# Kernel tuning notes

Measured on AMD Instinct MI355X. Metric: run time of the kernel, lower is better.

## Reference

```python
import jax, jax.numpy as jnp
import numpy as np

ANGLE_BITS = 3          # TurboQuantConfig.angle_bits default
LEVELS = 2 ** ANGLE_BITS
PI = np.pi


def _angle_ranges(d_minus_1, dtype):
    # hyperspherical coords: first d-2 angles in [0, pi], last angle in [0, 2*pi)
    return jnp.concatenate([
        jnp.full((d_minus_1 - 1,), PI, dtype),
        jnp.full((1,), 2.0 * PI, dtype),
    ])


def polar_compress(x):
    """x: [..., d] -> (r [...,1], theta_indices int32 [..., d-1])."""
    # suffix norms s_i = ||x[i:]|| via reversed cumsum of squares
    suffix = jnp.sqrt(jnp.cumsum((x * x)[..., ::-1], axis=-1)[..., ::-1])
    r = suffix[..., :1]
    cos_t = jnp.clip(x[..., :-1] / jnp.maximum(suffix[..., :-1], 1e-12), -1.0, 1.0)
    theta = jnp.arccos(cos_t)                      # [..., d-1], in [0, pi]
    # last angle carries the sign of x[..., -1]: map to [0, 2*pi)
    last = jnp.where(x[..., -1:] < 0, 2.0 * PI - theta[..., -1:], theta[..., -1:])
    theta = jnp.concatenate([theta[..., :-1], last], axis=-1)
    ranges = _angle_ranges(theta.shape[-1], theta.dtype)
    idx = jnp.round(theta / ranges * (LEVELS - 1)).astype(jnp.int32)
    return r, idx


def polar_decompress(r, idx):
    """(r [...,1], idx [..., d-1]) -> x_hat [..., d] via trig products."""
    d1 = idx.shape[-1]
    ranges = _angle_ranges(d1, r.dtype)
    theta = idx.astype(r.dtype) / (LEVELS - 1) * ranges
    sinp = jnp.cumprod(jnp.sin(theta), axis=-1)                 # [..., d-1]
    prods = jnp.concatenate([jnp.ones_like(r), sinp], axis=-1)  # [..., d]
    coss = jnp.concatenate([jnp.cos(theta), jnp.ones_like(r)], axis=-1)
    return r * prods * coss


def setup_inputs() -> dict:
    key = jax.random.key(0)
    kq, kk, kv, kn = jax.random.split(key, 4)
    B, H, T, k, d = 1, 32, 8192, 16, 128
    return {
        "queries": jax.random.normal(kq, (B, H, k, d), jnp.float32),
        "keys": jax.random.normal(kk, (B, H, T, d), jnp.float32),
        "values": jax.random.normal(kv, (B, H, T, d), jnp.float32),
        # faithful stand-in for `torch.randn_like(scores) * 0.01` QJL correction,
        # materialized deterministically as an input
        "qjl_noise": jax.random.normal(kn, (B, H, k, T), jnp.float32) * 0.01,
    }


def reference(queries, keys, values, qjl_noise):
    d = queries.shape[-1]
    # compress_kv_cache: polar angle quantization of keys and values
    r_k, idx_k = polar_compress(keys)
    r_v, idx_v = polar_compress(values)
    # compute_attention_with_compressed_kv: decompress-then-attend
    keys_polar = polar_decompress(r_k, idx_k)      # [B,H,T,d]
    values_polar = polar_decompress(r_v, idx_v)    # [B,H,T,d]
    scores = jnp.einsum('bhkd,bhtd->bhkt', queries, keys_polar) / jnp.sqrt(
        jnp.asarray(d, queries.dtype))
    scores = scores + qjl_noise
    attn = jax.nn.softmax(scores, axis=-1)
    return jnp.einsum('bhkt,bhtd->bhkd', attn, values_polar)
```

## Files before the change

kernel.cpp:

```cpp
#include <hip/hip_runtime.h>
#include <math.h>

typedef __attribute__((ext_vector_type(8))) short bf16x8;
typedef __attribute__((ext_vector_type(4))) float f32x4;
typedef __attribute__((ext_vector_type(2))) float f32x2;

#define HEADS 32
#define SEQT  8192
#define DIM   128
#define NQ    16
#define BPH   64
#define BTOK  128
#define WTOK  32
#define CHK   16
#define NPART BPH
#define PSTR  132
#define QSCALE 0.08838834764831845f

#define OFF_QS    0
#define OFF_PS    4096
#define OFF_KS    8192
#define OFF_ML    0
#define OFF_MERGE 8192
#define LDS_BYTES 24576

#define W1SQ 0.9504844339512096f
#define W2SQ 0.6112604669781572f
#define W3SQ 0.1882550990706332f
#define S1C  0.4338837391175581f
#define S2C  0.7818314824680298f
#define S3C  0.9749279121818236f
#define C1C  0.9009688679024191f
#define C2C  0.6234898018587336f
#define C3C  0.2225209339563144f
#define B1SQ 0.8117449009293667f
#define B2SQ 0.0495155660487913f
#define B3SQ 0.3887395330218429f

#define DPP_QP_XOR1 0xB1
#define DPP_QP_XOR2 0x4E
#define DPP_QP_SHL1 0x39
#define DPP_QP_SHR1 0x90
#define DPP_QP_SHR2 0x44
#define DPP_QP_BC0  0x00
#define DPP_QP_BC3  0xFF
#define DPP_HALF_MIRR 0x141
#define DPP_MIRR      0x140

template <int CTRL>
__device__ __forceinline__ float dpp0(float v) {
  return __int_as_float(__builtin_amdgcn_update_dpp(
      0, __float_as_int(v), CTRL, 0xF, 0xF, true));
}
__device__ __forceinline__ float rmax16(float v) {
  v = fmaxf(v, dpp0<DPP_QP_XOR1>(v));
  v = fmaxf(v, dpp0<DPP_QP_XOR2>(v));
  v = fmaxf(v, dpp0<DPP_HALF_MIRR>(v));
  v = fmaxf(v, dpp0<DPP_MIRR>(v));
  return v;
}
__device__ __forceinline__ float rsum16(float v) {
  v += dpp0<DPP_QP_XOR1>(v);
  v += dpp0<DPP_QP_XOR2>(v);
  v += dpp0<DPP_HALF_MIRR>(v);
  v += dpp0<DPP_MIRR>(v);
  return v;
}
__device__ __forceinline__ float rdlane(float v, int l) {
  return __int_as_float(__builtin_amdgcn_readlane(__float_as_int(v), l));
}
__device__ __forceinline__ unsigned short f2bf(float f) {
  unsigned u = __float_as_uint(f);
  u += 0x7FFFu + ((u >> 16) & 1u);
  return (unsigned short)(u >> 16);
}
__device__ __forceinline__ unsigned cvtpk(float lo, float hi) {
  unsigned r;
  asm("v_cvt_pk_bf16_f32 %0, %1, %2" : "=v"(r) : "v"(lo), "v"(hi));
  return r;
}

__device__ __forceinline__ void loadx(float x[16], const float* __restrict__ g, int lane) {
  const int tloc = lane >> 3;
  const int o    = lane & 7;
  const float4* p = (const float4*)(g + tloc * DIM + o * 16);
  const float4 a = p[0], b = p[1], c = p[2], d = p[3];
  x[0]=a.x;  x[1]=a.y;  x[2]=a.z;  x[3]=a.w;
  x[4]=b.x;  x[5]=b.y;  x[6]=b.z;  x[7]=b.w;
  x[8]=c.x;  x[9]=c.y;  x[10]=c.z; x[11]=c.w;
  x[12]=d.x; x[13]=d.y; x[14]=d.z; x[15]=d.w;
}

template <bool KOUT>
__device__ __forceinline__ void decomp8(
    const float (&x)[16], int lane,
    unsigned short* KsW, float* VsW, int q8)
{
  const int tloc = lane >> 3;
  const int o    = lane & 7;

  float qa0 = 0.f, qa1 = 0.f;
#pragma unroll
  for (int i = 0; i < 16; i += 2) {
    qa0 = fmaf(x[i], x[i], qa0);
    qa1 = fmaf(x[i+1], x[i+1], qa1);
  }
  const float qs = qa0 + qa1;
  const float a1 = dpp0<DPP_QP_SHL1>(qs);
  const float t1 = qs + (((lane & 3) == 3) ? 0.f : a1);
  const float b1 = dpp0<DPP_QP_XOR2>(t1);
  const float t2 = t1 + (((lane & 3) < 2) ? b1 : 0.f);
  const float qt = dpp0<DPP_QP_BC0>(t2);
  const float ot = dpp0<DPP_HALF_MIRR>(qt);
  const float total = qt + ot;
  const float S = t2 + ((o < 4) ? ot : 0.f);

  const float r = sqrtf(total);

  float run = S, psin = 1.f, run14 = 0.f;
  float sv[16], cv[16];
#pragma unroll
  for (int i = 0; i < 16; ++i) {
    const float u = x[i] * x[i];
    if (i == 14) run14 = run;
    const bool lo2 = u < W2SQ * run;
    const float thr = lo2 ? W3SQ : W1SQ;
    const bool bx = u < thr * run;
    const float ssin = lo2 ? (bx ? S3C : S2C) : (bx ? S1C : 0.f);
    float scos = lo2 ? (bx ? C3C : C2C) : (bx ? C1C : 1.f);
    scos = copysignf(scos, x[i]);
    sv[i] = ssin; cv[i] = scos;
    psin *= ssin;
    run -= u;
  }
  const float p1 = dpp0<DPP_QP_SHR1>(psin);
  const float e1 = psin * (((lane & 3) == 0) ? 1.f : p1);
  const float p2 = dpp0<DPP_QP_SHR2>(e1);
  const float e2 = e1 * (((lane & 3) < 2) ? 1.f : p2);
  const float pq = dpp0<DPP_QP_BC3>(e2);
  const float po = dpp0<DPP_HALF_MIRR>(pq);
  const float e3 = e2 * ((o >= 4) ? po : 1.f);
  const float sh = dpp0<DPP_QP_SHR1>(e3);
  const float E = ((lane & 3) == 0) ? ((o < 4) ? 1.f : po) : sh;

  float rcum = r * E;
  const int T = q8 * 8 + tloc;
#pragma unroll
  for (int g = 0; g < 2; ++g) {
    float outv[8];
    float rc14 = rcum;
#pragma unroll
    for (int k = 0; k < 8; ++k) {
      const int i = 8 * g + k;
      if (i == 14) rc14 = rcum;
      outv[k] = rcum * cv[i];
      rcum *= sv[i];
    }
    if (g == 1) {
      const float u14 = x[14] * x[14];
      const bool neg = x[14] < 0.f;
      const bool cc1 = u14 < B1SQ * run14;
      const bool cc2 = u14 < B2SQ * run14;
      const bool cc3 = u14 > B3SQ * run14;
      const float cpos = cc2 ? -C3C : (cc1 ? C2C : 1.f);
      const float spos = cc2 ? S3C : (cc1 ? S2C : 0.f);
      const float cneg = cc3 ? -C1C : -C3C;
      const float sneg = cc3 ? S1C : S3C;
      const float cB = neg ? cneg : cpos;
      float sB = neg ? sneg : spos;
      sB = copysignf(sB, x[15]);
      const bool o7 = (o == 7);
      outv[6] = o7 ? rc14 * cB : outv[6];
      outv[7] = o7 ? rc14 * sB : outv[7];
    }
    if (KOUT) {
      uint4 w;
      w.x = cvtpk(outv[0], outv[1]);
      w.y = cvtpk(outv[2], outv[3]);
      w.z = cvtpk(outv[4], outv[5]);
      w.w = cvtpk(outv[6], outv[7]);
      *(uint4*)&KsW[T * 128 + ((o * 16 + 8 * g) ^ (tloc << 3))] = w;
    } else {
      const int f0 = (o * 16 + 8 * g) ^ (tloc << 2);
      *(float4*)&VsW[tloc * 128 + f0]       = make_float4(outv[0], outv[1], outv[2], outv[3]);
      *(float4*)&VsW[tloc * 128 + (f0 ^ 4)] = make_float4(outv[4], outv[5], outv[6], outv[7]);
    }
  }
}

__global__ __launch_bounds__(256, 2)
void attn_partial(const float* __restrict__ Q, const float* __restrict__ K,
                  const float* __restrict__ V, const float* __restrict__ noise,
                  float* __restrict__ part) {
  __shared__ __align__(16) char RAW[LDS_BYTES];
  unsigned short* Qs = (unsigned short*)(RAW + OFF_QS);
  float*          Ps = (float*)(RAW + OFF_PS);
  float2*         Ml = (float2*)(RAW + OFF_ML);

  const int tid  = threadIdx.x;
  const int lane = tid & 63;
  const int wv   = tid >> 6;
  const int h    = blockIdx.x / BPH;
  const int bh   = blockIdx.x % BPH;
  const int r16  = lane & 15, G = lane >> 4;

  unsigned short* KsW = (unsigned short*)(RAW + OFF_KS + wv * 4096);
  float* VsW = (float*)KsW;
  float* myP = Ps + wv * (CHK * NQ);

  const size_t hoff = (size_t)h * SEQT * DIM;
  const int t0 = bh * BTOK + wv * WTOK;
  const float* Kg = K + hoff + (size_t)t0 * DIM;
  const float* Vg = V + hoff + (size_t)t0 * DIM;

  float xa[16], xb[16];
  loadx(xa, Kg, lane);
  {
    const float* Qh = Q + (size_t)h * NQ * DIM;
    for (int i = tid; i < NQ * DIM; i += 256)
      Qs[i] = f2bf(Qh[i] * QSCALE);
  }
  __syncthreads();

  bf16x8 qa[4];
#pragma unroll
  for (int c = 0; c < 4; ++c)
    qa[c] = *(const bf16x8*)&Qs[r16 * 128 + c * 32 + G * 8];

  f32x2 acc[NQ];
#pragma unroll
  for (int qq = 0; qq < NQ; ++qq) acc[qq] = (f32x2){0.f, 0.f};
  float m_r[4] = {-INFINITY, -INFINITY, -INFINITY, -INFINITY};
  float l_r[4] = {0.f, 0.f, 0.f, 0.f};

  const float* nh = noise + (size_t)h * NQ * SEQT + t0 + r16;

#pragma unroll 1
  for (int ch = 0; ch < 2; ++ch) {
    const float* KgC = Kg + ch * 2048;
    const float* VgC = Vg + ch * 2048;

    loadx(xb, KgC + 1024, lane);
    decomp8<true>(xa, lane, KsW, VsW, 0);
    loadx(xa, VgC, lane);
    decomp8<true>(xb, lane, KsW, VsW, 1);

    f32x4 d0 = {0.f, 0.f, 0.f, 0.f};
#pragma unroll
    for (int c = 0; c < 4; ++c) {
      bf16x8 b0 = *(const bf16x8*)&KsW[r16 * 128 + ((c * 32 + G * 8) ^ ((r16 & 7) << 3))];
      d0 = __builtin_amdgcn_mfma_f32_16x16x32_bf16(qa[c], b0, d0, 0, 0, 0);
    }
    const float* nt = nh + ch * CHK;
    float s0_[4];
#pragma unroll
    for (int rr = 0; rr < 4; ++rr)
      s0_[rr] = d0[rr] + nt[(size_t)(4 * G + rr) * SEQT];
    float al_r[4];
#pragma unroll
    for (int rr = 0; rr < 4; ++rr) {
      float mt = rmax16(s0_[rr]);
      float mn = fmaxf(m_r[rr], mt);
      al_r[rr] = __expf(m_r[rr] - mn);
      m_r[rr] = mn;
    }
    float p0[4];
#pragma unroll
    for (int rr = 0; rr < 4; ++rr) {
      p0[rr] = __expf(s0_[rr] - m_r[rr]);
      l_r[rr] = l_r[rr] * al_r[rr] + rsum16(p0[rr]);
    }
    *(float4*)&myP[r16 * NQ + 4 * G] = make_float4(p0[0], p0[1], p0[2], p0[3]);
#pragma unroll
    for (int qq = 0; qq < NQ; ++qq) {
      float alq = rdlane(al_r[qq & 3], (qq >> 2) << 4);
      acc[qq] *= (f32x2){alq, alq};
    }

    loadx(xb, VgC + 1024, lane);
#pragma unroll 1
    for (int sc = 0; sc < 2; ++sc) {
      decomp8<false>(sc == 0 ? xa : xb, lane, KsW, VsW, 0);
      if (sc == 0 && ch == 0)
        loadx(xa, KgC + 2048, lane);
#pragma unroll 2
      for (int tt = 0; tt < 8; ++tt) {
        float2 vh = *(const float2*)&VsW[tt * 128 + ((2 * lane) ^ (tt << 2))];
        f32x2 vh2 = {vh.x, vh.y};
        const float* pv = &myP[(sc * 8 + tt) * NQ];
        float4 pa = ((const float4*)pv)[0];
        float4 pb = ((const float4*)pv)[1];
        float4 pc = ((const float4*)pv)[2];
        float4 pd = ((const float4*)pv)[3];
        float pq[NQ] = {pa.x, pa.y, pa.z, pa.w, pb.x, pb.y, pb.z, pb.w,
                        pc.x, pc.y, pc.z, pc.w, pd.x, pd.y, pd.z, pd.w};
#pragma unroll
        for (int qq = 0; qq < NQ; ++qq)
          acc[qq] = __builtin_elementwise_fma((f32x2){pq[qq], pq[qq]}, vh2, acc[qq]);
      }
    }
  }

  if (r16 == 0) {
#pragma unroll
    for (int rr = 0; rr < 4; ++rr)
      Ml[wv * NQ + 4 * G + rr] = make_float2(m_r[rr], l_r[rr]);
  }
  __syncthreads();
#pragma unroll
  for (int qq = 0; qq < NQ; ++qq) {
    float2 e0 = Ml[0 * NQ + qq], e1 = Ml[1 * NQ + qq];
    float2 e2 = Ml[2 * NQ + qq], e3 = Ml[3 * NQ + qq];
    float Mq = fmaxf(fmaxf(e0.x, e1.x), fmaxf(e2.x, e3.x));
    float own = (wv == 0) ? e0.x : ((wv == 1) ? e1.x : ((wv == 2) ? e2.x : e3.x));
    float al = __expf(own - Mq);
    acc[qq] *= (f32x2){al, al};
  }
  float* buf = (float*)(RAW + OFF_MERGE);
  if (wv >= 2) {
#pragma unroll
    for (int qq = 0; qq < NQ; ++qq)
      *(float2*)&buf[(wv - 2) * 2048 + qq * 128 + 2 * lane] =
          make_float2(acc[qq].x, acc[qq].y);
  }
  __syncthreads();
  if (wv < 2) {
#pragma unroll
    for (int qq = 0; qq < NQ; ++qq) {
      float2 t = *(const float2*)&buf[wv * 2048 + qq * 128 + 2 * lane];
      acc[qq] += (f32x2){t.x, t.y};
    }
  }
  __syncthreads();
  if (wv == 1) {
#pragma unroll
    for (int qq = 0; qq < NQ; ++qq)
      *(float2*)&buf[qq * 128 + 2 * lane] = make_float2(acc[qq].x, acc[qq].y);
  }
  __syncthreads();
  if (wv == 0) {
    float* P = part + ((size_t)h * NPART + bh) * (NQ * PSTR);
#pragma unroll
    for (int qq = 0; qq < NQ; ++qq) {
      float2 t = *(const float2*)&buf[qq * 128 + 2 * lane];
      *(float2*)&P[qq * PSTR + 4 + 2 * lane] =
          make_float2(acc[qq].x + t.x, acc[qq].y + t.y);
      float2 e0 = Ml[0 * NQ + qq], e1 = Ml[1 * NQ + qq];
      float2 e2 = Ml[2 * NQ + qq], e3 = Ml[3 * NQ + qq];
      float Mq = fmaxf(fmaxf(e0.x, e1.x), fmaxf(e2.x, e3.x));
      float Lq = e0.y * __expf(e0.x - Mq) + e1.y * __expf(e1.x - Mq) +
                 e2.y * __expf(e2.x - Mq) + e3.y * __expf(e3.x - Mq);
      if (lane == 0) *(float2*)&P[qq * PSTR] = make_float2(Mq, Lq);
    }
  }
}

__global__ __launch_bounds__(128)
void attn_reduce(const float* __restrict__ part, float* __restrict__ out) {
  __shared__ float wgt[NPART];
  __shared__ float Lsh;
  const int tid = threadIdx.x;
  const int h = blockIdx.x >> 4;
  const int q = blockIdx.x & 15;
  const float* P = part + (size_t)h * NPART * NQ * PSTR;
  if (tid < NPART) {
    float2 ml = *(const float2*)&P[((size_t)tid * NQ + q) * PSTR];
    float M = ml.x;
#pragma unroll
    for (int off = 1; off < 64; off <<= 1)
      M = fmaxf(M, __shfl_xor(M, off, 64));
    float w = __expf(ml.x - M);
    wgt[tid] = w;
    float L = ml.y * w;
#pragma unroll
    for (int off = 1; off < 64; off <<= 1)
      L += __shfl_xor(L, off, 64);
    if (tid == 0) Lsh = L;
  }
  __syncthreads();
  const float* A = P + (size_t)q * PSTR + 4 + tid;
  float o = 0.f;
#pragma unroll 8
  for (int c = 0; c < NPART; ++c)
    o = fmaf(wgt[c], A[(size_t)c * NQ * PSTR], o);
  out[((size_t)h * NQ + q) * DIM + tid] = o * (1.0f / Lsh);
}

extern "C" void kernel_launch(void* const* d_in, const int* in_sizes, int n_in,
                              void* d_out, int out_size, void* d_ws, size_t ws_size,
                              hipStream_t stream) {
  (void)in_sizes; (void)n_in; (void)out_size; (void)ws_size;
  const float* Q = (const float*)d_in[0];
  const float* K = (const float*)d_in[1];
  const float* V = (const float*)d_in[2];
  const float* noise = (const float*)d_in[3];
  float* part = (float*)d_ws;
  attn_partial<<<dim3(HEADS * BPH), dim3(256), 0, stream>>>(Q, K, V, noise, part);
  attn_reduce<<<dim3(HEADS * NQ), dim3(128), 0, stream>>>(part, (float*)d_out);
}
```

Before: 309.5 us.

## Compute P·V with bf16 MFMA over the full 32-token wave tile

Replaces the scalar fp32 FMA P·V accumulation with a bf16 MFMA: values are decompressed into a transposed, swizzled bf16 LDS tile and the probabilities are packed to bf16. Each wave now scores all 32 tokens up front, does a single softmax pass without online rescaling, and then runs 8 MFMAs for the output. LDS grows from 24 KB to 65 KB per block, which may reduce occupancy below the two blocks per CU the launch bounds request. Rounding probabilities and values to bf16 also lowers accuracy.

```diff
diff --git a/kernel.cpp b/kernel.cpp
--- a/kernel.cpp
+++ b/kernel.cpp
@@ -2,8 +2,8 @@
 #include <math.h>
 
 typedef __attribute__((ext_vector_type(8))) short bf16x8;
+typedef __attribute__((ext_vector_type(4))) short bf16x4;
 typedef __attribute__((ext_vector_type(4))) float f32x4;
-typedef __attribute__((ext_vector_type(2))) float f32x2;
 
 #define HEADS 32
 #define SEQT  8192
@@ -12,17 +12,17 @@
 #define BPH   64
 #define BTOK  128
 #define WTOK  32
-#define CHK   16
 #define NPART BPH
 #define PSTR  132
 #define QSCALE 0.08838834764831845f
 
 #define OFF_QS    0
-#define OFF_PS    4096
-#define OFF_KS    8192
+#define OFF_PL    4096
+#define OFF_KS    9216
+#define OFF_VS    25600
 #define OFF_ML    0
-#define OFF_MERGE 8192
-#define LDS_BYTES 24576
+#define OFF_MERGE 9216
+#define LDS_BYTES 66560
 
 #define W1SQ 0.9504844339512096f
 #define W2SQ 0.6112604669781572f
@@ -66,9 +66,6 @@
   v += dpp0<DPP_MIRR>(v);
   return v;
 }
-__device__ __forceinline__ float rdlane(float v, int l) {
-  return __int_as_float(__builtin_amdgcn_readlane(__float_as_int(v), l));
-}
 __device__ __forceinline__ unsigned short f2bf(float f) {
   unsigned u = __float_as_uint(f);
   u += 0x7FFFu + ((u >> 16) & 1u);
@@ -94,7 +91,7 @@
 template <bool KOUT>
 __device__ __forceinline__ void decomp8(
     const float (&x)[16], int lane,
-    unsigned short* KsW, float* VsW, int q8)
+    unsigned short* KsW, unsigned short* Vl, int tbase)
 {
   const int tloc = lane >> 3;
   const int o    = lane & 7;
@@ -144,7 +141,7 @@
   const float E = ((lane & 3) == 0) ? ((o < 4) ? 1.f : po) : sh;
 
   float rcum = r * E;
-  const int T = q8 * 8 + tloc;
+  const int T = tbase + tloc;
 #pragma unroll
   for (int g = 0; g < 2; ++g) {
     float outv[8];
@@ -179,11 +176,15 @@
       w.y = cvtpk(outv[2], outv[3]);
       w.z = cvtpk(outv[4], outv[5]);
       w.w = cvtpk(outv[6], outv[7]);
-      *(uint4*)&KsW[T * 128 + ((o * 16 + 8 * g) ^ (tloc << 3))] = w;
+      *(uint4*)&KsW[(T & 15) * 128 + ((o * 16 + 8 * g) ^ (tloc << 3))] = w;
     } else {
-      const int f0 = (o * 16 + 8 * g) ^ (tloc << 2);
-      *(float4*)&VsW[tloc * 128 + f0]       = make_float4(outv[0], outv[1], outv[2], outv[3]);
-      *(float4*)&VsW[tloc * 128 + (f0 ^ 4)] = make_float4(outv[4], outv[5], outv[6], outv[7]);
+      const int ps = T ^ (o << 2);
+#pragma unroll
+      for (int k = 0; k < 8; k += 2) {
+        const unsigned u = cvtpk(outv[k], outv[k+1]);
+        Vl[(o * 16 + 8 * g + k)     * 40 + ps] = (unsigned short)u;
+        Vl[(o * 16 + 8 * g + k + 1) * 40 + ps] = (unsigned short)(u >> 16);
+      }
     }
   }
 }
@@ -194,7 +195,6 @@
                   float* __restrict__ part) {
   __shared__ __align__(16) char RAW[LDS_BYTES];
   unsigned short* Qs = (unsigned short*)(RAW + OFF_QS);
-  float*          Ps = (float*)(RAW + OFF_PS);
   float2*         Ml = (float2*)(RAW + OFF_ML);
 
   const int tid  = threadIdx.x;
@@ -204,9 +204,9 @@
   const int bh   = blockIdx.x % BPH;
   const int r16  = lane & 15, G = lane >> 4;
 
-  unsigned short* KsW = (unsigned short*)(RAW + OFF_KS + wv * 4096);
-  float* VsW = (float*)KsW;
-  float* myP = Ps + wv * (CHK * NQ);
+  unsigned short* Pl  = (unsigned short*)(RAW + OFF_PL) + wv * 640;
+  unsigned short* KsW = (unsigned short*)(RAW + OFF_KS) + wv * 2048;
+  unsigned short* Vl  = (unsigned short*)(RAW + OFF_VS) + wv * 5120;
 
   const size_t hoff = (size_t)h * SEQT * DIM;
   const int t0 = bh * BTOK + wv * WTOK;
@@ -227,124 +227,132 @@
   for (int c = 0; c < 4; ++c)
     qa[c] = *(const bf16x8*)&Qs[r16 * 128 + c * 32 + G * 8];
 
-  f32x2 acc[NQ];
-#pragma unroll
-  for (int qq = 0; qq < NQ; ++qq) acc[qq] = (f32x2){0.f, 0.f};
-  float m_r[4] = {-INFINITY, -INFINITY, -INFINITY, -INFINITY};
-  float l_r[4] = {0.f, 0.f, 0.f, 0.f};
-
   const float* nh = noise + (size_t)h * NQ * SEQT + t0 + r16;
 
-#pragma unroll 1
-  for (int ch = 0; ch < 2; ++ch) {
-    const float* KgC = Kg + ch * 2048;
-    const float* VgC = Vg + ch * 2048;
-
-    loadx(xb, KgC + 1024, lane);
-    decomp8<true>(xa, lane, KsW, VsW, 0);
-    loadx(xa, VgC, lane);
-    decomp8<true>(xb, lane, KsW, VsW, 1);
-
-    f32x4 d0 = {0.f, 0.f, 0.f, 0.f};
-#pragma unroll
-    for (int c = 0; c < 4; ++c) {
-      bf16x8 b0 = *(const bf16x8*)&KsW[r16 * 128 + ((c * 32 + G * 8) ^ ((r16 & 7) << 3))];
-      d0 = __builtin_amdgcn_mfma_f32_16x16x32_bf16(qa[c], b0, d0, 0, 0, 0);
-    }
-    const float* nt = nh + ch * CHK;
-    float s0_[4];
+  loadx(xb, Kg + 1024, lane);
+  decomp8<true>(xa, lane, KsW, Vl, 0);
+  loadx(xa, Kg + 2048, lane);
+  decomp8<true>(xb, lane, KsW, Vl, 8);
+
+  f32x4 dA = {0.f, 0.f, 0.f, 0.f};
+#pragma unroll
+  for (int c = 0; c < 4; ++c) {
+    bf16x8 b0 = *(const bf16x8*)&KsW[r16 * 128 + ((c * 32 + G * 8) ^ ((r16 & 7) << 3))];
+    dA = __builtin_amdgcn_mfma_f32_16x16x32_bf16(qa[c], b0, dA, 0, 0, 0);
+  }
+  float sA[4];
+#pragma unroll
+  for (int rr = 0; rr < 4; ++rr)
+    sA[rr] = dA[rr] + nh[(size_t)(4 * G + rr) * SEQT];
+
+  loadx(xb, Kg + 3072, lane);
+  decomp8<true>(xa, lane, KsW, Vl, 0);
+  loadx(xa, Vg, lane);
+  decomp8<true>(xb, lane, KsW, Vl, 8);
+
+  f32x4 dB = {0.f, 0.f, 0.f, 0.f};
+#pragma unroll
+  for (int c = 0; c < 4; ++c) {
+    bf16x8 b0 = *(const bf16x8*)&KsW[r16 * 128 + ((c * 32 + G * 8) ^ ((r16 & 7) << 3))];
+    dB = __builtin_amdgcn_mfma_f32_16x16x32_bf16(qa[c], b0, dB, 0, 0, 0);
+  }
+  float sB[4];
+#pragma unroll
+  for (int rr = 0; rr < 4; ++rr)
+    sB[rr] = dB[rr] + nh[(size_t)(4 * G + rr) * SEQT + 16];
+
+  float mt[4], l_r[4];
+#pragma unroll
+  for (int rr = 0; rr < 4; ++rr) {
+    mt[rr] = fmaxf(rmax16(sA[rr]), rmax16(sB[rr]));
+    const float pA = __expf(sA[rr] - mt[rr]);
+    const float pB = __expf(sB[rr] - mt[rr]);
+    l_r[rr] = rsum16(pA) + rsum16(pB);
+    const unsigned u = cvtpk(pA, pB);
+    Pl[(4 * G + rr) * 40 + r16]      = (unsigned short)u;
+    Pl[(4 * G + rr) * 40 + 16 + r16] = (unsigned short)(u >> 16);
+  }
+
+  loadx(xb, Vg + 1024, lane);
+  decomp8<false>(xa, lane, KsW, Vl, 0);
+  loadx(xa, Vg + 2048, lane);
+  decomp8<false>(xb, lane, KsW, Vl, 8);
+  loadx(xb, Vg + 3072, lane);
+  decomp8<false>(xa, lane, KsW, Vl, 16);
+  decomp8<false>(xb, lane, KsW, Vl, 24);
+
+  const bf16x8 pf = *(const bf16x8*)&Pl[r16 * 40 + 8 * G];
+  f32x4 acc[8];
+#pragma unroll
+  for (int dt = 0; dt < 8; ++dt) acc[dt] = (f32x4){0.f, 0.f, 0.f, 0.f};
+#pragma unroll
+  for (int dt = 0; dt < 8; ++dt) {
+    const int gb = G ^ (dt >> 1);
+    const int sw = (dt & 1) << 2;
+    const unsigned short* vr = &Vl[(dt * 16 + r16) * 40 + 8 * gb];
+    const bf16x4 v0 = *(const bf16x4*)&vr[sw];
+    const bf16x4 v1 = *(const bf16x4*)&vr[4 - sw];
+    const bf16x8 vf = __builtin_shufflevector(v0, v1, 0, 1, 2, 3, 4, 5, 6, 7);
+    acc[dt] = __builtin_amdgcn_mfma_f32_16x16x32_bf16(pf, vf, acc[dt], 0, 0, 0);
+  }
+
+  if (r16 == 0) {
 #pragma unroll
     for (int rr = 0; rr < 4; ++rr)
-      s0_[rr] = d0[rr] + nt[(size_t)(4 * G + rr) * SEQT];
-    float al_r[4];
-#pragma unroll
-    for (int rr = 0; rr < 4; ++rr) {
-      float mt = rmax16(s0_[rr]);
-      float mn = fmaxf(m_r[rr], mt);
-      al_r[rr] = __expf(m_r[rr] - mn);
-      m_r[rr] = mn;
-    }
-    float p0[4];
-#pragma unroll
-    for (int rr = 0; rr < 4; ++rr) {
-      p0[rr] = __expf(s0_[rr] - m_r[rr]);
-      l_r[rr] = l_r[rr] * al_r[rr] + rsum16(p0[rr]);
-    }
-    *(float4*)&myP[r16 * NQ + 4 * G] = make_float4(p0[0], p0[1], p0[2], p0[3]);
-#pragma unroll
-    for (int qq = 0; qq < NQ; ++qq) {
-      float alq = rdlane(al_r[qq & 3], (qq >> 2) << 4);
-      acc[qq] *= (f32x2){alq, alq};
-    }
-
-    loadx(xb, VgC + 1024, lane);
-#pragma unroll 1
-    for (int sc = 0; sc < 2; ++sc) {
-      decomp8<false>(sc == 0 ? xa : xb, lane, KsW, VsW, 0);
-      if (sc == 0 && ch == 0)
-        loadx(xa, KgC + 2048, lane);
-#pragma unroll 2
-      for (int tt = 0; tt < 8; ++tt) {
-        float2 vh = *(const float2*)&VsW[tt * 128 + ((2 * lane) ^ (tt << 2))];
-        f32x2 vh2 = {vh.x, vh.y};
-        const float* pv = &myP[(sc * 8 + tt) * NQ];
-        float4 pa = ((const float4*)pv)[0];
-        float4 pb = ((const float4*)pv)[1];
-        float4 pc = ((const float4*)pv)[2];
-        float4 pd = ((const float4*)pv)[3];
-        float pq[NQ] = {pa.x, pa.y, pa.z, pa.w, pb.x, pb.y, pb.z, pb.w,
-                        pc.x, pc.y, pc.z, pc.w, pd.x, pd.y, pd.z, pd.w};
-#pragma unroll
-        for (int qq = 0; qq < NQ; ++qq)
-          acc[qq] = __builtin_elementwise_fma((f32x2){pq[qq], pq[qq]}, vh2, acc[qq]);
-      }
-    }
-  }
-
-  if (r16 == 0) {
-#pragma unroll
-    for (int rr = 0; rr < 4; ++rr)
-      Ml[wv * NQ + 4 * G + rr] = make_float2(m_r[rr], l_r[rr]);
-  }
-  __syncthreads();
-#pragma unroll
-  for (int qq = 0; qq < NQ; ++qq) {
-    float2 e0 = Ml[0 * NQ + qq], e1 = Ml[1 * NQ + qq];
-    float2 e2 = Ml[2 * NQ + qq], e3 = Ml[3 * NQ + qq];
+      Ml[wv * NQ + 4 * G + rr] = make_float2(mt[rr], l_r[rr]);
+  }
+  __syncthreads();
+  float al[4];
+#pragma unroll
+  for (int reg = 0; reg < 4; ++reg) {
+    const int q = 4 * G + reg;
+    float2 e0 = Ml[0 * NQ + q], e1 = Ml[1 * NQ + q];
+    float2 e2 = Ml[2 * NQ + q], e3 = Ml[3 * NQ + q];
     float Mq = fmaxf(fmaxf(e0.x, e1.x), fmaxf(e2.x, e3.x));
     float own = (wv == 0) ? e0.x : ((wv == 1) ? e1.x : ((wv == 2) ? e2.x : e3.x));
-    float al = __expf(own - Mq);
-    acc[qq] *= (f32x2){al, al};
-  }
+    al[reg] = __expf(own - Mq);
+  }
+#pragma unroll
+  for (int dt = 0; dt < 8; ++dt)
+#pragma unroll
+    for (int reg = 0; reg < 4; ++reg) acc[dt][reg] *= al[reg];
+
   float* buf = (float*)(RAW + OFF_MERGE);
   if (wv >= 2) {
 #pragma unroll
-    for (int qq = 0; qq < NQ; ++qq)
-      *(float2*)&buf[(wv - 2) * 2048 + qq * 128 + 2 * lane] =
-          make_float2(acc[qq].x, acc[qq].y);
+    for (int dt = 0; dt < 8; ++dt)
+#pragma unroll
+      for (int reg = 0; reg < 4; ++reg)
+        buf[(wv - 2) * 2112 + (4 * G + reg) * 132 + dt * 16 + r16] = acc[dt][reg];
   }
   __syncthreads();
   if (wv < 2) {
 #pragma unroll
-    for (int qq = 0; qq < NQ; ++qq) {
-      float2 t = *(const float2*)&buf[wv * 2048 + qq * 128 + 2 * lane];
-      acc[qq] += (f32x2){t.x, t.y};
-    }
+    for (int dt = 0; dt < 8; ++dt)
+#pragma unroll
+      for (int reg = 0; reg < 4; ++reg)
+        acc[dt][reg] += buf[wv * 2112 + (4 * G + reg) * 132 + dt * 16 + r16];
   }
   __syncthreads();
   if (wv == 1) {
 #pragma unroll
-    for (int qq = 0; qq < NQ; ++qq)
-      *(float2*)&buf[qq * 128 + 2 * lane] = make_float2(acc[qq].x, acc[qq].y);
+    for (int dt = 0; dt < 8; ++dt)
+#pragma unroll
+      for (int reg = 0; reg < 4; ++reg)
+        buf[(4 * G + reg) * 132 + dt * 16 + r16] = acc[dt][reg];
   }
   __syncthreads();
   if (wv == 0) {
     float* P = part + ((size_t)h * NPART + bh) * (NQ * PSTR);
 #pragma unroll
+    for (int dt = 0; dt < 8; ++dt)
+#pragma unroll
+      for (int reg = 0; reg < 4; ++reg) {
+        const int q = 4 * G + reg, d = dt * 16 + r16;
+        P[q * PSTR + 4 + d] = acc[dt][reg] + buf[q * 132 + d];
+      }
+#pragma unroll
     for (int qq = 0; qq < NQ; ++qq) {
-      float2 t = *(const float2*)&buf[qq * 128 + 2 * lane];
-      *(float2*)&P[qq * PSTR + 4 + 2 * lane] =
-          make_float2(acc[qq].x + t.x, acc[qq].y + t.y);
       float2 e0 = Ml[0 * NQ + qq], e1 = Ml[1 * NQ + qq];
       float2 e2 = Ml[2 * NQ + qq], e3 = Ml[3 * NQ + qq];
       float Mq = fmaxf(fmaxf(e0.x, e1.x), fmaxf(e2.x, e3.x));
```

Measured after the change: 300.2 us. -3.0%, faster.
